# Kernel optimization log

Hardware: AMD Instinct MI355X
Metric: run time of the kernel (lower is better)

The kernel has to match this reference:

```python
import jax, jax.numpy as jnp
import numpy as np

D = 256; NH = 8; NL = 4; NP = 4; DH = D // NH; DFFN = 1024; NQ = 900; BS = 4
SPATIAL = ((92, 92), (46, 46), (23, 23), (12, 12))  # (H, W) per level
LEVEL_START = (0, 8464, 10580, 11109)
S = sum(h * w for h, w in SPATIAL)  # 11253


def _ln(x, g, b):
    m = jnp.mean(x, -1, keepdims=True)
    v = jnp.var(x, -1, keepdims=True)
    return (x - m) / jnp.sqrt(v + 1e-5) * g + b


def setup_inputs() -> dict:
    key = jax.random.key(0)
    ks = jax.random.split(key, 24)
    p = lambda k, s: 0.02 * jax.random.normal(k, s, jnp.float32)
    return {
        "tgt": jax.random.normal(ks[0], (NQ, BS, D), jnp.float32),
        "tgt_query_pos": jax.random.normal(ks[1], (NQ, BS, D), jnp.float32),
        "tgt_reference_points": jax.random.uniform(ks[2], (NQ, BS, NL, 2), jnp.float32),
        "memory": jax.random.normal(ks[3], (S, BS, D), jnp.float32),
        "memory_spatial_shapes": jnp.array(SPATIAL, jnp.int32),
        "memory_level_start_index": jnp.array(LEVEL_START, jnp.int32),
        "in_proj_w": p(ks[4], (3 * D, D)), "in_proj_b": p(ks[5], (3 * D,)),
        "out_proj_w": p(ks[6], (D, D)), "out_proj_b": p(ks[7], (D,)),
        "off_w": p(ks[8], (NH * NL * NP * 2, D)), "off_b": p(ks[9], (NH * NL * NP * 2,)),
        "aw_w": p(ks[10], (NH * NL * NP, D)), "aw_b": p(ks[11], (NH * NL * NP,)),
        "vproj_w": p(ks[12], (D, D)), "vproj_b": p(ks[13], (D,)),
        "oproj_w": p(ks[14], (D, D)), "oproj_b": p(ks[15], (D,)),
        "ln1_g": jnp.ones((D,), jnp.float32), "ln1_b": jnp.zeros((D,), jnp.float32),
        "ln2_g": jnp.ones((D,), jnp.float32), "ln2_b": jnp.zeros((D,), jnp.float32),
        "ln3_g": jnp.ones((D,), jnp.float32), "ln3_b": jnp.zeros((D,), jnp.float32),
        "lin1_w": p(ks[16], (DFFN, D)), "lin1_b": p(ks[17], (DFFN,)),
        "lin2_w": p(ks[18], (D, DFFN)), "lin2_b": p(ks[19], (D,)),
    }


def _self_attn(q, k, v, in_w, in_b, out_w, out_b):
    # q, k, v: (nq, bs, d) -- torch nn.MultiheadAttention, eval mode
    wq, wk, wv = jnp.split(in_w, 3, axis=0)
    bq, bk, bv = jnp.split(in_b, 3)
    qp = (q @ wq.T + bq).reshape(NQ, BS, NH, DH)
    kp = (k @ wk.T + bk).reshape(NQ, BS, NH, DH)
    vp = (v @ wv.T + bv).reshape(NQ, BS, NH, DH)
    s = jnp.einsum("qbhd,kbhd->bhqk", qp, kp) / jnp.sqrt(jnp.float32(DH))
    a = jax.nn.softmax(s, axis=-1)
    o = jnp.einsum("bhqk,kbhd->qbhd", a, vp).reshape(NQ, BS, D)
    return o @ out_w.T + out_b


def _msdeform(x, ref, mem, off_w, off_b, aw_w, aw_b, vproj_w, vproj_b, oproj_w, oproj_b):
    # x: (bs, nq, d); ref: (bs, nq, nl, 2) in [0,1]; mem: (bs, S, d)
    value = (mem @ vproj_w.T + vproj_b).reshape(BS, S, NH, DH)
    off = (x @ off_w.T + off_b).reshape(BS, NQ, NH, NL, NP, 2)
    aw = jax.nn.softmax((x @ aw_w.T + aw_b).reshape(BS, NQ, NH, NL * NP), axis=-1)
    aw = aw.reshape(BS, NQ, NH, NL, NP)
    # offset normalizer = (W, H) per level
    norm = jnp.array([[w, h] for (h, w) in SPATIAL], jnp.float32)
    loc = ref[:, :, None, :, None, :] + off / norm[None, None, None, :, None, :]
    out = jnp.zeros((BS, NH, NQ, DH), x.dtype)
    for l, (H, W) in enumerate(SPATIAL):
        s0 = LEVEL_START[l]
        v = value[:, s0:s0 + H * W].transpose(0, 2, 1, 3)  # (bs, nh, H*W, dh)
        g = loc[:, :, :, l].transpose(0, 2, 1, 3, 4)       # (bs, nh, nq, np, 2)
        # grid_sample align_corners=False, padding_mode='zeros'
        px = g[..., 0] * W - 0.5
        py = g[..., 1] * H - 0.5
        x0 = jnp.floor(px).astype(jnp.int32)
        y0 = jnp.floor(py).astype(jnp.int32)
        wx = px - x0
        wy = py - y0
        samp = jnp.zeros((BS, NH, NQ, NP, DH), x.dtype)
        for dx, dy, w in ((0, 0, (1 - wx) * (1 - wy)), (1, 0, wx * (1 - wy)),
                          (0, 1, (1 - wx) * wy), (1, 1, wx * wy)):
            xi = x0 + dx
            yi = y0 + dy
            valid = ((xi >= 0) & (xi < W) & (yi >= 0) & (yi < H)).astype(x.dtype)
            idx = (jnp.clip(yi, 0, H - 1) * W + jnp.clip(xi, 0, W - 1)).reshape(BS, NH, NQ * NP)
            gat = jnp.take_along_axis(v, idx[..., None], axis=2).reshape(BS, NH, NQ, NP, DH)
            samp = samp + (w * valid)[..., None] * gat
        a = aw[:, :, :, l].transpose(0, 2, 1, 3)  # (bs, nh, nq, np)
        out = out + (samp * a[..., None]).sum(axis=3)
    out = out.transpose(0, 2, 1, 3).reshape(BS, NQ, D)
    return out @ oproj_w.T + oproj_b


def reference(tgt, tgt_query_pos, tgt_reference_points, memory,
              memory_spatial_shapes, memory_level_start_index,
              in_proj_w, in_proj_b, out_proj_w, out_proj_b,
              off_w, off_b, aw_w, aw_b, vproj_w, vproj_b, oproj_w, oproj_b,
              ln1_g, ln1_b, ln2_g, ln2_b, ln3_g, ln3_b,
              lin1_w, lin1_b, lin2_w, lin2_b):
    # module_seq = ['sa', 'ca', 'ffn']; dropout inactive (eval)
    q = tgt + tgt_query_pos
    tgt2 = _self_attn(q, q, tgt, in_proj_w, in_proj_b, out_proj_w, out_proj_b)
    tgt = _ln(tgt + tgt2, ln2_g, ln2_b)
    x = (tgt + tgt_query_pos).transpose(1, 0, 2)
    ref = tgt_reference_points.transpose(1, 0, 2, 3)
    mem = memory.transpose(1, 0, 2)
    tgt2 = _msdeform(x, ref, mem, off_w, off_b, aw_w, aw_b,
                     vproj_w, vproj_b, oproj_w, oproj_b).transpose(1, 0, 2)
    tgt = _ln(tgt + tgt2, ln1_g, ln1_b)
    ff = jax.nn.relu(tgt @ lin1_w.T + lin1_b) @ lin2_w.T + lin2_b
    return _ln(tgt + ff, ln3_g, ln3_b)
```

## Files before the change

### kernel.cpp

```cpp
#include <hip/hip_runtime.h>
#include <math.h>

#define D_MODEL 256
#define NHEAD   8
#define NLVL    4
#define NPTS    4
#define DHEAD   32
#define DFFN    1024
#define NQ      900
#define BSZ     4
#define NROW    (NQ * BSZ)
#define S_TOT   11253
#define VROWS   (S_TOT * BSZ)
#define SASCALE 0.17677669529663687f

typedef __attribute__((ext_vector_type(8))) short short8;
typedef __attribute__((ext_vector_type(4))) float f32x4;
typedef unsigned short ushort_t;

static __device__ __forceinline__ unsigned f2bf1(float f) {
    unsigned u = __float_as_uint(f);
    return (u + 0x7FFFu + ((u >> 16) & 1u)) >> 16;
}
static __device__ __forceinline__ unsigned pack2bf(float x, float y) {
    return f2bf1(x) | (f2bf1(y) << 16);
}
static __device__ __forceinline__ float bf2f(ushort_t u) {
    return __uint_as_float(((unsigned)u) << 16);
}

#define GPAD 72

__global__ __launch_bounds__(256) void qkv_fused(
    const float* __restrict__ tgt, const float* __restrict__ qpos,
    const float* __restrict__ W, const float* __restrict__ bias,
    ushort_t* __restrict__ C)
{
    __shared__ ushort_t As[64 * GPAD];
    __shared__ ushort_t Ws[64 * GPAD];

    const int t  = threadIdx.x;
    const int m0 = blockIdx.x * 64;
    const int n0 = blockIdx.y * 64;
    const bool addpos = (n0 < 512);
    const float oscale = (n0 < 256) ? SASCALE : 1.f;

    const int trow = t >> 2;
    const int tk   = (t & 3) << 4;
    const int wv   = t >> 6;
    const int ln   = t & 63;
    const int L    = ln & 15;
    const int quad = ln >> 4;

    f32x4 acc[4] = {{0.f,0.f,0.f,0.f},{0.f,0.f,0.f,0.f},
                    {0.f,0.f,0.f,0.f},{0.f,0.f,0.f,0.f}};

    for (int k0 = 0; k0 < 256; k0 += 64) {
        {
            int m = m0 + trow;
            float4 a0, a1, a2, a3;
            if (m < NROW) {
                const float* ap = tgt + (size_t)m * 256 + k0 + tk;
                a0 = *(const float4*)(ap + 0);
                a1 = *(const float4*)(ap + 4);
                a2 = *(const float4*)(ap + 8);
                a3 = *(const float4*)(ap + 12);
                if (addpos) {
                    const float* pp = qpos + (size_t)m * 256 + k0 + tk;
                    float4 p0 = *(const float4*)(pp + 0);
                    float4 p1 = *(const float4*)(pp + 4);
                    float4 p2 = *(const float4*)(pp + 8);
                    float4 p3 = *(const float4*)(pp + 12);
                    a0.x += p0.x; a0.y += p0.y; a0.z += p0.z; a0.w += p0.w;
                    a1.x += p1.x; a1.y += p1.y; a1.z += p1.z; a1.w += p1.w;
                    a2.x += p2.x; a2.y += p2.y; a2.z += p2.z; a2.w += p2.w;
                    a3.x += p3.x; a3.y += p3.y; a3.z += p3.z; a3.w += p3.w;
                }
            } else {
                a0 = a1 = a2 = a3 = make_float4(0.f, 0.f, 0.f, 0.f);
            }
            uint4 u0, u1;
            u0.x = pack2bf(a0.x, a0.y); u0.y = pack2bf(a0.z, a0.w);
            u0.z = pack2bf(a1.x, a1.y); u0.w = pack2bf(a1.z, a1.w);
            u1.x = pack2bf(a2.x, a2.y); u1.y = pack2bf(a2.z, a2.w);
            u1.z = pack2bf(a3.x, a3.y); u1.w = pack2bf(a3.z, a3.w);
            *(uint4*)&As[trow * GPAD + tk + 0] = u0;
            *(uint4*)&As[trow * GPAD + tk + 8] = u1;
        }
        {
            int n = n0 + trow;
            const float* wp = W + (size_t)n * 256 + k0 + tk;
            float4 a0 = *(const float4*)(wp + 0);
            float4 a1 = *(const float4*)(wp + 4);
            float4 a2 = *(const float4*)(wp + 8);
            float4 a3 = *(const float4*)(wp + 12);
            uint4 u0, u1;
            u0.x = pack2bf(a0.x, a0.y); u0.y = pack2bf(a0.z, a0.w);
            u0.z = pack2bf(a1.x, a1.y); u0.w = pack2bf(a1.z, a1.w);
            u1.x = pack2bf(a2.x, a2.y); u1.y = pack2bf(a2.z, a2.w);
            u1.z = pack2bf(a3.x, a3.y); u1.w = pack2bf(a3.z, a3.w);
            *(uint4*)&Ws[trow * GPAD + tk + 0] = u0;
            *(uint4*)&Ws[trow * GPAD + tk + 8] = u1;
        }
        __syncthreads();
#pragma unroll
        for (int kh = 0; kh < 2; ++kh) {
            short8 af = *(const short8*)&As[(wv * 16 + L) * GPAD + kh * 32 + quad * 8];
#pragma unroll
            for (int cb = 0; cb < 4; ++cb) {
                short8 bf = *(const short8*)&Ws[(cb * 16 + L) * GPAD + kh * 32 + quad * 8];
                acc[cb] = __builtin_amdgcn_mfma_f32_16x16x32_bf16(af, bf, acc[cb], 0, 0, 0);
            }
        }
        __syncthreads();
    }
#pragma unroll
    for (int cb = 0; cb < 4; ++cb) {
        int col = n0 + cb * 16 + L;
        float bv = bias[col];
#pragma unroll
        for (int i = 0; i < 4; ++i) {
            int m = m0 + wv * 16 + quad * 4 + i;
            if (m < NROW)
                C[(size_t)m * 768 + col] = (ushort_t)f2bf1((acc[cb][i] + bv) * oscale);
        }
    }
}

__global__ __launch_bounds__(256) void sa_flash16(
    const ushort_t* __restrict__ qkv, ushort_t* __restrict__ attn_out)
{
    __shared__ ushort_t Ks[2 * 2080];
    __shared__ ushort_t Vt[2 * 2304];
    __shared__ ushort_t Ps[4 * 1152];

    const int t    = threadIdx.x;
    const int q0   = blockIdx.x * 64;
    const int b    = blockIdx.y & 3;
    const int h    = blockIdx.y >> 2;
// ... 182 lines not shown
        __syncthreads();
    }
#pragma unroll
    for (int cb = 0; cb < 4; ++cb) {
        int col = n0 + cb * 16 + L;
        float bv = bias[col];
#pragma unroll
        for (int i = 0; i < 4; ++i) {
            int m = m0 + wv * 16 + quad * 4 + i;
            if (m < M)
                C[(size_t)m * ldc + col] = acc[cb][i] + bv;
        }
    }
}

__global__ __launch_bounds__(256) void ln_resid16(
    const float* __restrict__ xa, const float* __restrict__ xb,
    const float* __restrict__ gam, const float* __restrict__ bet,
    float* __restrict__ out, const float* __restrict__ pos,
    ushort_t* __restrict__ out2)
{
    const int row = blockIdx.x;
    const int t = threadIdx.x;
    float x = xa[(size_t)row * D_MODEL + t] + xb[(size_t)row * D_MODEL + t];
    float s = x, s2 = x * x;
#pragma unroll
    for (int off = 32; off > 0; off >>= 1) {
        s  += __shfl_down(s, off, 64);
        s2 += __shfl_down(s2, off, 64);
    }
    __shared__ float rs[4], rs2[4];
    __shared__ float mean_s, rstd_s;
    int wid = t >> 6, lane = t & 63;
    if (lane == 0) { rs[wid] = s; rs2[wid] = s2; }
    __syncthreads();
    if (t == 0) {
        float S = rs[0] + rs[1] + rs[2] + rs[3];
        float S2 = rs2[0] + rs2[1] + rs2[2] + rs2[3];
        float mean = S * (1.f / 256.f);
        float var = S2 * (1.f / 256.f) - mean * mean;
        mean_s = mean;
        rstd_s = rsqrtf(var + 1e-5f);
    }
    __syncthreads();
    float y = (x - mean_s) * rstd_s * gam[t] + bet[t];
    out[(size_t)row * D_MODEL + t] = y;
    if (out2) {
        float o2 = y + (pos ? pos[(size_t)row * D_MODEL + t] : 0.f);
        out2[(size_t)row * D_MODEL + t] = (ushort_t)f2bf1(o2);
    }
}

__global__ __launch_bounds__(256) void vproj_bf16(
    const float* __restrict__ A, const float* __restrict__ W,
    const float* __restrict__ bias, ushort_t* __restrict__ C, int M)
{
    __shared__ ushort_t As[64 * GPAD];
    __shared__ ushort_t Ws[256 * GPAD];

    const int t  = threadIdx.x;
    const int m0 = blockIdx.x * 64;
    const int trow = t >> 2;
    const int tk   = (t & 3) << 4;
    const int wv   = t >> 6;
    const int ln   = t & 63;
    const int L    = ln & 15;
    const int quad = ln >> 4;

    f32x4 acc[16];
#pragma unroll
    for (int i = 0; i < 16; ++i) acc[i] = (f32x4){0.f, 0.f, 0.f, 0.f};

    for (int k0 = 0; k0 < 256; k0 += 64) {
        {
            int m = m0 + trow;
            float4 a0, a1, a2, a3;
            if (m < M) {
                const float* ap = A + (size_t)m * 256 + k0 + tk;
                a0 = *(const float4*)(ap + 0);
                a1 = *(const float4*)(ap + 4);
                a2 = *(const float4*)(ap + 8);
                a3 = *(const float4*)(ap + 12);
            } else {
                a0 = a1 = a2 = a3 = make_float4(0.f, 0.f, 0.f, 0.f);
            }
            uint4 u0, u1;
            u0.x = pack2bf(a0.x, a0.y); u0.y = pack2bf(a0.z, a0.w);
            u0.z = pack2bf(a1.x, a1.y); u0.w = pack2bf(a1.z, a1.w);
            u1.x = pack2bf(a2.x, a2.y); u1.y = pack2bf(a2.z, a2.w);
            u1.z = pack2bf(a3.x, a3.y); u1.w = pack2bf(a3.z, a3.w);
            *(uint4*)&As[trow * GPAD + tk + 0] = u0;
            *(uint4*)&As[trow * GPAD + tk + 8] = u1;
        }
#pragma unroll
        for (int wb = 0; wb < 4; ++wb) {
            int n = wb * 64 + trow;
            const float* wp = W + (size_t)n * 256 + k0 + tk;
            float4 a0 = *(const float4*)(wp + 0);
            float4 a1 = *(const float4*)(wp + 4);
            float4 a2 = *(const float4*)(wp + 8);
            float4 a3 = *(const float4*)(wp + 12);
            uint4 u0, u1;
            u0.x = pack2bf(a0.x, a0.y); u0.y = pack2bf(a0.z, a0.w);
            u0.z = pack2bf(a1.x, a1.y); u0.w = pack2bf(a1.z, a1.w);
            u1.x = pack2bf(a2.x, a2.y); u1.y = pack2bf(a2.z, a2.w);
            u1.z = pack2bf(a3.x, a3.y); u1.w = pack2bf(a3.z, a3.w);
            *(uint4*)&Ws[n * GPAD + tk + 0] = u0;
            *(uint4*)&Ws[n * GPAD + tk + 8] = u1;
        }
        __syncthreads();
#pragma unroll
        for (int kh = 0; kh < 2; ++kh) {
            short8 af = *(const short8*)&As[(wv * 16 + L) * GPAD + kh * 32 + quad * 8];
#pragma unroll
            for (int cb = 0; cb < 16; ++cb) {
                short8 bf = *(const short8*)&Ws[(cb * 16 + L) * GPAD + kh * 32 + quad * 8];
                acc[cb] = __builtin_amdgcn_mfma_f32_16x16x32_bf16(af, bf, acc[cb], 0, 0, 0);
            }
        }
        __syncthreads();
    }

    ushort_t* Cs = Ws;
#pragma unroll
    for (int cb = 0; cb < 16; ++cb) {
        int col = cb * 16 + L;
        float bv = bias[col];
#pragma unroll
        for (int i = 0; i < 4; ++i) {
            int r = wv * 16 + quad * 4 + i;
            Cs[r * 264 + col] = (ushort_t)f2bf1(acc[cb][i] + bv);
        }
    }
    __syncthreads();
    {
        int r  = t >> 2;
        int ch = (t & 3) * 64;
        int m  = m0 + r;
        if (m < M) {
            const ushort_t* src = &Cs[r * 264 + ch];
            uint4* dst = (uint4*)(C + (size_t)m * 256 + ch);
#pragma unroll
            for (int j = 0; j < 8; ++j)
                dst[j] = *(const uint4*)(src + j * 8);
        }
    }
}

__global__ __launch_bounds__(256) void offaw16(
    const ushort_t* __restrict__ A,
    const float* __restrict__ off_w, const float* __restrict__ off_b,
    const float* __restrict__ aw_w, const float* __restrict__ aw_b,
    float* __restrict__ off_raw, float* __restrict__ aw_raw)
{
    __shared__ ushort_t As[64 * GPAD];
    __shared__ ushort_t Ws[64 * GPAD];

    const int t  = threadIdx.x;
    const int m0 = blockIdx.x * 64;
    const int by = blockIdx.y;
    const bool isaw = (by >= 4);
    const int n0 = isaw ? (by - 4) * 64 : by * 64;
    const float* W  = isaw ? aw_w : off_w;
    const float* bs = isaw ? aw_b : off_b;
    float* C = isaw ? aw_raw : off_raw;
    const int ldc = isaw ? 128 : 256;

    const int trow = t >> 2;
    const int tk   = (t & 3) << 4;
    const int wv   = t >> 6;
    const int ln   = t & 63;
    const int L    = ln & 15;
    const int quad = ln >> 4;

    f32x4 acc[4] = {{0.f,0.f,0.f,0.f},{0.f,0.f,0.f,0.f},
                    {0.f,0.f,0.f,0.f},{0.f,0.f,0.f,0.f}};

    for (int k0 = 0; k0 < 256; k0 += 64) {
        {
            int m = m0 + trow;
            uint4 a0 = make_uint4(0u,0u,0u,0u), a1 = make_uint4(0u,0u,0u,0u);
            if (m < NROW) {
                const ushort_t* ap = A + (size_t)m * 256 + k0 + tk;
                a0 = *(const uint4*)ap;
                a1 = *(const uint4*)(ap + 8);
            }
            *(uint4*)&As[trow * GPAD + tk + 0] = a0;
            *(uint4*)&As[trow * GPAD + tk + 8] = a1;
        }
        {
            int n = n0 + trow;
            const float* wp = W + (size_t)n * 256 + k0 + tk;
            float4 a0 = *(const float4*)(wp + 0);
            float4 a1 = *(const float4*)(wp + 4);
            float4 a2 = *(const float4*)(wp + 8);
            float4 a3 = *(const float4*)(wp + 12);
            uint4 u0, u1;
            u0.x = pack2bf(a0.x, a0.y); u0.y = pack2bf(a0.z, a0.w);
            u0.z = pack2bf(a1.x, a1.y); u0.w = pack2bf(a1.z, a1.w);
            u1.x = pack2bf(a2.x, a2.y); u1.y = pack2bf(a2.z, a2.w);
            u1.z = pack2bf(a3.x, a3.y); u1.w = pack2bf(a3.z, a3.w);
            *(uint4*)&Ws[trow * GPAD + tk + 0] = u0;
            *(uint4*)&Ws[trow * GPAD + tk + 8] = u1;
        }
        __syncthreads();
#pragma unroll
        for (int kh = 0; kh < 2; ++kh) {
            short8 af = *(const short8*)&As[(wv * 16 + L) * GPAD + kh * 32 + quad * 8];
#pragma unroll
            for (int cb = 0; cb < 4; ++cb) {
                short8 bf = *(const short8*)&Ws[(cb * 16 + L) * GPAD + kh * 32 + quad * 8];
                acc[cb] = __builtin_amdgcn_mfma_f32_16x16x32_bf16(af, bf, acc[cb], 0, 0, 0);
            }
        }
        __syncthreads();
    }
#pragma unroll
    for (int cb = 0; cb < 4; ++cb) {
        int col = n0 + cb * 16 + L;
        float bv = bs[col];
#pragma unroll
        for (int i = 0; i < 4; ++i) {
            int m = m0 + wv * 16 + quad * 4 + i;
            if (m < NROW)
                C[(size_t)m * ldc + col] = acc[cb][i] + bv;
        }
    }
}

__global__ __launch_bounds__(256) void gemm16_16(
    const ushort_t* __restrict__ A, const float* __restrict__ W,
    const float* __restrict__ bias, ushort_t* __restrict__ C,
    int M, int N, int K, int ldc, int relu)
{
    __shared__ ushort_t As[64 * GPAD];
    __shared__ ushort_t Ws[64 * GPAD];

    const int t  = threadIdx.x;
    const int m0 = blockIdx.x * 64;
    const int n0 = blockIdx.y * 64;
    const int trow = t >> 2;
    const int tk   = (t & 3) << 4;
    const int wv   = t >> 6;
    const int ln   = t & 63;
    const int L    = ln & 15;
    const int quad = ln >> 4;

    f32x4 acc[4] = {{0.f,0.f,0.f,0.f},{0.f,0.f,0.f,0.f},
                    {0.f,0.f,0.f,0.f},{0.f,0.f,0.f,0.f}};

    for (int k0 = 0; k0 < K; k0 += 64) {
        {
            int m = m0 + trow;
            uint4 a0 = make_uint4(0u,0u,0u,0u), a1 = make_uint4(0u,0u,0u,0u);
            if (m < M) {
                const ushort_t* ap = A + (size_t)m * K + k0 + tk;
                a0 = *(const uint4*)ap;
                a1 = *(const uint4*)(ap + 8);
            }
            *(uint4*)&As[trow * GPAD + tk + 0] = a0;
            *(uint4*)&As[trow * GPAD + tk + 8] = a1;
        }
        {
            int n = n0 + trow;
            const float* wp = W + (size_t)n * K + k0 + tk;
            float4 a0 = *(const float4*)(wp + 0);
            float4 a1 = *(const float4*)(wp + 4);
            float4 a2 = *(const float4*)(wp + 8);
            float4 a3 = *(const float4*)(wp + 12);
            uint4 u0, u1;
            u0.x = pack2bf(a0.x, a0.y); u0.y = pack2bf(a0.z, a0.w);
            u0.z = pack2bf(a1.x, a1.y); u0.w = pack2bf(a1.z, a1.w);
            u1.x = pack2bf(a2.x, a2.y); u1.y = pack2bf(a2.z, a2.w);
            u1.z = pack2bf(a3.x, a3.y); u1.w = pack2bf(a3.z, a3.w);
            *(uint4*)&Ws[trow * GPAD + tk + 0] = u0;
            *(uint4*)&Ws[trow * GPAD + tk + 8] = u1;
        }
        __syncthreads();
#pragma unroll
        for (int kh = 0; kh < 2; ++kh) {
            short8 af = *(const short8*)&As[(wv * 16 + L) * GPAD + kh * 32 + quad * 8];
#pragma unroll
            for (int cb = 0; cb < 4; ++cb) {
                short8 bf = *(const short8*)&Ws[(cb * 16 + L) * GPAD + kh * 32 + quad * 8];
                acc[cb] = __builtin_amdgcn_mfma_f32_16x16x32_bf16(af, bf, acc[cb], 0, 0, 0);
            }
        }
        __syncthreads();
    }
#pragma unroll
    for (int cb = 0; cb < 4; ++cb) {
        int col = n0 + cb * 16 + L;
        float bv = bias[col];
#pragma unroll
        for (int i = 0; i < 4; ++i) {
            int m = m0 + wv * 16 + quad * 4 + i;
            if (m < M) {
                float o = acc[cb][i] + bv;
                if (relu) o = fmaxf(o, 0.f);
                C[(size_t)m * ldc + col] = (ushort_t)f2bf1(o);
            }
        }
    }
}

__global__ __launch_bounds__(256) void msdeform16(
    const float* __restrict__ off_raw, const float* __restrict__ aw_raw,
    const float* __restrict__ refp, const ushort_t* __restrict__ value,
    ushort_t* __restrict__ out)
{
    const int row = blockIdx.x;
    const int b = row & 3;
    const int t = threadIdx.x;

    __shared__ float aw_s[8][17];
    __shared__ float px_s[8][16];
    __shared__ float py_s[8][16];

// ... 82 lines not shown
    const float* op_w   = (const float*)d_in[16];
    const float* op_b   = (const float*)d_in[17];
    const float* ln1g   = (const float*)d_in[18];
    const float* ln1b   = (const float*)d_in[19];
    const float* ln2g   = (const float*)d_in[20];
    const float* ln2b   = (const float*)d_in[21];
    const float* ln3g   = (const float*)d_in[22];
    const float* ln3b   = (const float*)d_in[23];
    const float* l1w    = (const float*)d_in[24];
    const float* l1b    = (const float*)d_in[25];
    const float* l2w    = (const float*)d_in[26];
    const float* l2b    = (const float*)d_in[27];
    float* out = (float*)d_out;
    float* ws  = (float*)d_ws;

    ushort_t* qkv16   = (ushort_t*)ws;
    ushort_t* att16   = (ushort_t*)(ws + 1382400);
    float*    tgt_a   = ws + 1843200;
    ushort_t* xca16   = (ushort_t*)(ws + 2764800);
    float*    off_raw = ws + 3225600;
    float*    aw_raw  = ws + 4147200;
    ushort_t* att2_16 = (ushort_t*)(ws + 4608000);
    float*    tgt_b   = ws + 5068800;
    ushort_t* tgtb16  = (ushort_t*)(ws + 5990400);
    ushort_t* value16 = (ushort_t*)(ws + 6451200);
    ushort_t* hidden16= (ushort_t*)(ws + 12212736);
    float*    tmp     = ws + 14055936;

    dim3 b256(256);

    hipLaunchKernelGGL(qkv_fused, dim3(57, 12), b256, 0, stream,
                       tgt, qpos, in_w, in_b, qkv16);
    hipLaunchKernelGGL(sa_flash16, dim3(15, 32), b256, 0, stream, qkv16, att16);
    hipLaunchKernelGGL(gemm16_f32, dim3(57, 4), b256, 0, stream,
                       att16, outp_w, outp_b, tmp, NROW, 256, 256, 256);
    hipLaunchKernelGGL(ln_resid16, dim3(3600), b256, 0, stream,
                       tgt, tmp, ln2g, ln2b, tgt_a, qpos, xca16);
    hipLaunchKernelGGL(vproj_bf16, dim3(704), b256, 0, stream,
                       mem, vp_w, vp_b, value16, VROWS);
    hipLaunchKernelGGL(offaw16, dim3(57, 6), b256, 0, stream,
                       xca16, off_w, off_b, aw_w, aw_b, off_raw, aw_raw);
    hipLaunchKernelGGL(msdeform16, dim3(3600), b256, 0, stream,
                       off_raw, aw_raw, refp, value16, att2_16);
    hipLaunchKernelGGL(gemm16_f32, dim3(57, 4), b256, 0, stream,
                       att2_16, op_w, op_b, tmp, NROW, 256, 256, 256);
    hipLaunchKernelGGL(ln_resid16, dim3(3600), b256, 0, stream,
                       tgt_a, tmp, ln1g, ln1b, tgt_b, (const float*)nullptr, tgtb16);
    hipLaunchKernelGGL(gemm16_16, dim3(57, 16), b256, 0, stream,
                       tgtb16, l1w, l1b, hidden16, NROW, 1024, 256, 1024, 1);
    hipLaunchKernelGGL(gemm16_f32, dim3(57, 4), b256, 0, stream,
                       hidden16, l2w, l2b, tmp, NROW, 256, 1024, 256);
    hipLaunchKernelGGL(ln_resid16, dim3(3600), b256, 0, stream,
                       tgt_b, tmp, ln3g, ln3b, out, (const float*)nullptr, (ushort_t*)nullptr);
}
```

Measured before the change: 290.9 us.

## Fuse QKV and value projections; fold LayerNorms into following GEMM prologues

Merges the QKV projection and the memory value projection into one launch, with the block index picking which GEMM a block runs. The LayerNorm after self-attention is fused into the offset/attention-weight GEMM, and the LayerNorm after cross-attention is fused into the first FFN GEMM. Each GEMM block computes the row LN itself and stages the normalized bf16 rows in shared memory, removing two kernel launches and the intermediate bf16 buffers. In exchange, the LN is recomputed by every column block (6x and 16x redundant reads of tgt and tmp), and the fused kernels use more shared memory.

```diff
diff --git a/kernel.cpp b/kernel.cpp
--- a/kernel.cpp
+++ b/kernel.cpp
@@ -31,20 +31,18 @@
 
 #define GPAD 72
 
-__global__ __launch_bounds__(256) void qkv_fused(
+__global__ __launch_bounds__(256) void proj_fused(
     const float* __restrict__ tgt, const float* __restrict__ qpos,
-    const float* __restrict__ W, const float* __restrict__ bias,
-    ushort_t* __restrict__ C)
+    const float* __restrict__ in_w, const float* __restrict__ in_b,
+    const float* __restrict__ mem, const float* __restrict__ vp_w,
+    const float* __restrict__ vp_b,
+    ushort_t* __restrict__ qkv16, ushort_t* __restrict__ value16)
 {
     __shared__ ushort_t As[64 * GPAD];
-    __shared__ ushort_t Ws[64 * GPAD];
-
-    const int t  = threadIdx.x;
-    const int m0 = blockIdx.x * 64;
-    const int n0 = blockIdx.y * 64;
-    const bool addpos = (n0 < 512);
-    const float oscale = (n0 < 256) ? SASCALE : 1.f;
-
+    __shared__ ushort_t Ws[256 * GPAD];
+
+    const int t    = threadIdx.x;
+    const int bid  = blockIdx.x;
     const int trow = t >> 2;
     const int tk   = (t & 3) << 4;
     const int wv   = t >> 6;
@@ -52,77 +50,165 @@
     const int L    = ln & 15;
     const int quad = ln >> 4;
 
-    f32x4 acc[4] = {{0.f,0.f,0.f,0.f},{0.f,0.f,0.f,0.f},
-                    {0.f,0.f,0.f,0.f},{0.f,0.f,0.f,0.f}};
-
-    for (int k0 = 0; k0 < 256; k0 += 64) {
+    if (bid < 684) {
+        const int m0 = (bid % 57) * 64;
+        const int n0 = (bid / 57) * 64;
+        const bool addpos = (n0 < 512);
+        const float oscale = (n0 < 256) ? SASCALE : 1.f;
+
+        f32x4 acc[4] = {{0.f,0.f,0.f,0.f},{0.f,0.f,0.f,0.f},
+                        {0.f,0.f,0.f,0.f},{0.f,0.f,0.f,0.f}};
+
+        for (int k0 = 0; k0 < 256; k0 += 64) {
+            {
+                int m = m0 + trow;
+                float4 a0, a1, a2, a3;
+                if (m < NROW) {
+                    const float* ap = tgt + (size_t)m * 256 + k0 + tk;
+                    a0 = *(const float4*)(ap + 0);
+                    a1 = *(const float4*)(ap + 4);
+                    a2 = *(const float4*)(ap + 8);
+                    a3 = *(const float4*)(ap + 12);
+                    if (addpos) {
+                        const float* pp = qpos + (size_t)m * 256 + k0 + tk;
+                        float4 p0 = *(const float4*)(pp + 0);
+                        float4 p1 = *(const float4*)(pp + 4);
+                        float4 p2 = *(const float4*)(pp + 8);
+                        float4 p3 = *(const float4*)(pp + 12);
+                        a0.x += p0.x; a0.y += p0.y; a0.z += p0.z; a0.w += p0.w;
+                        a1.x += p1.x; a1.y += p1.y; a1.z += p1.z; a1.w += p1.w;
+                        a2.x += p2.x; a2.y += p2.y; a2.z += p2.z; a2.w += p2.w;
+                        a3.x += p3.x; a3.y += p3.y; a3.z += p3.z; a3.w += p3.w;
+                    }
+                } else {
+                    a0 = a1 = a2 = a3 = make_float4(0.f, 0.f, 0.f, 0.f);
+                }
+                uint4 u0, u1;
+                u0.x = pack2bf(a0.x, a0.y); u0.y = pack2bf(a0.z, a0.w);
+                u0.z = pack2bf(a1.x, a1.y); u0.w = pack2bf(a1.z, a1.w);
+                u1.x = pack2bf(a2.x, a2.y); u1.y = pack2bf(a2.z, a2.w);
+                u1.z = pack2bf(a3.x, a3.y); u1.w = pack2bf(a3.z, a3.w);
+                *(uint4*)&As[trow * GPAD + tk + 0] = u0;
+                *(uint4*)&As[trow * GPAD + tk + 8] = u1;
+            }
+            {
+                int n = n0 + trow;
+                const float* wp = in_w + (size_t)n * 256 + k0 + tk;
+                float4 a0 = *(const float4*)(wp + 0);
+                float4 a1 = *(const float4*)(wp + 4);
+                float4 a2 = *(const float4*)(wp + 8);
+                float4 a3 = *(const float4*)(wp + 12);
+                uint4 u0, u1;
+                u0.x = pack2bf(a0.x, a0.y); u0.y = pack2bf(a0.z, a0.w);
+                u0.z = pack2bf(a1.x, a1.y); u0.w = pack2bf(a1.z, a1.w);
+                u1.x = pack2bf(a2.x, a2.y); u1.y = pack2bf(a2.z, a2.w);
+                u1.z = pack2bf(a3.x, a3.y); u1.w = pack2bf(a3.z, a3.w);
+                *(uint4*)&Ws[trow * GPAD + tk + 0] = u0;
+                *(uint4*)&Ws[trow * GPAD + tk + 8] = u1;
+            }
+            __syncthreads();
+#pragma unroll
+            for (int kh = 0; kh < 2; ++kh) {
+                short8 af = *(const short8*)&As[(wv * 16 + L) * GPAD + kh * 32 + quad * 8];
+#pragma unroll
+                for (int cb = 0; cb < 4; ++cb) {
+                    short8 bf = *(const short8*)&Ws[(cb * 16 + L) * GPAD + kh * 32 + quad * 8];
+                    acc[cb] = __builtin_amdgcn_mfma_f32_16x16x32_bf16(af, bf, acc[cb], 0, 0, 0);
+                }
+            }
+            __syncthreads();
+        }
+#pragma unroll
+        for (int cb = 0; cb < 4; ++cb) {
+            int col = n0 + cb * 16 + L;
+            float bv = in_b[col];
+#pragma unroll
+            for (int i = 0; i < 4; ++i) {
+                int m = m0 + wv * 16 + quad * 4 + i;
+                if (m < NROW)
+                    qkv16[(size_t)m * 768 + col] = (ushort_t)f2bf1((acc[cb][i] + bv) * oscale);
+            }
+        }
+    } else {
+        const int m0 = (bid - 684) * 64;
+
+        f32x4 acc[16];
+#pragma unroll
+        for (int i = 0; i < 16; ++i) acc[i] = (f32x4){0.f, 0.f, 0.f, 0.f};
+
+        for (int k0 = 0; k0 < 256; k0 += 64) {
+            {
+                int m = m0 + trow;
+                float4 a0, a1, a2, a3;
+                if (m < VROWS) {
+                    const float* ap = mem + (size_t)m * 256 + k0 + tk;
+                    a0 = *(const float4*)(ap + 0);
+                    a1 = *(const float4*)(ap + 4);
+                    a2 = *(const float4*)(ap + 8);
+                    a3 = *(const float4*)(ap + 12);
+                } else {
+                    a0 = a1 = a2 = a3 = make_float4(0.f, 0.f, 0.f, 0.f);
+                }
+                uint4 u0, u1;
+                u0.x = pack2bf(a0.x, a0.y); u0.y = pack2bf(a0.z, a0.w);
+                u0.z = pack2bf(a1.x, a1.y); u0.w = pack2bf(a1.z, a1.w);
+                u1.x = pack2bf(a2.x, a2.y); u1.y = pack2bf(a2.z, a2.w);
+                u1.z = pack2bf(a3.x, a3.y); u1.w = pack2bf(a3.z, a3.w);
+                *(uint4*)&As[trow * GPAD + tk + 0] = u0;
+                *(uint4*)&As[trow * GPAD + tk + 8] = u1;
+            }
+#pragma unroll
+            for (int wb = 0; wb < 4; ++wb) {
+                int n = wb * 64 + trow;
+                const float* wp = vp_w + (size_t)n * 256 + k0 + tk;
+                float4 a0 = *(const float4*)(wp + 0);
+                float4 a1 = *(const float4*)(wp + 4);
+                float4 a2 = *(const float4*)(wp + 8);
+                float4 a3 = *(const float4*)(wp + 12);
+                uint4 u0, u1;
+                u0.x = pack2bf(a0.x, a0.y); u0.y = pack2bf(a0.z, a0.w);
+                u0.z = pack2bf(a1.x, a1.y); u0.w = pack2bf(a1.z, a1.w);
+                u1.x = pack2bf(a2.x, a2.y); u1.y = pack2bf(a2.z, a2.w);
+                u1.z = pack2bf(a3.x, a3.y); u1.w = pack2bf(a3.z, a3.w);
+                *(uint4*)&Ws[n * GPAD + tk + 0] = u0;
+                *(uint4*)&Ws[n * GPAD + tk + 8] = u1;
+            }
+            __syncthreads();
+#pragma unroll
+            for (int kh = 0; kh < 2; ++kh) {
+                short8 af = *(const short8*)&As[(wv * 16 + L) * GPAD + kh * 32 + quad * 8];
+#pragma unroll
+                for (int cb = 0; cb < 16; ++cb) {
+                    short8 bf = *(const short8*)&Ws[(cb * 16 + L) * GPAD + kh * 32 + quad * 8];
+                    acc[cb] = __builtin_amdgcn_mfma_f32_16x16x32_bf16(af, bf, acc[cb], 0, 0, 0);
+                }
+            }
+            __syncthreads();
+        }
+
+        ushort_t* Cs = Ws;
+#pragma unroll
+        for (int cb = 0; cb < 16; ++cb) {
+            int col = cb * 16 + L;
+            float bv = vp_b[col];
+#pragma unroll
+            for (int i = 0; i < 4; ++i) {
+                int r = wv * 16 + quad * 4 + i;
+                Cs[r * 264 + col] = (ushort_t)f2bf1(acc[cb][i] + bv);
+            }
+        }
+        __syncthreads();
         {
-            int m = m0 + trow;
-            float4 a0, a1, a2, a3;
-            if (m < NROW) {
-                const float* ap = tgt + (size_t)m * 256 + k0 + tk;
-                a0 = *(const float4*)(ap + 0);
-                a1 = *(const float4*)(ap + 4);
-                a2 = *(const float4*)(ap + 8);
-                a3 = *(const float4*)(ap + 12);
-                if (addpos) {
-                    const float* pp = qpos + (size_t)m * 256 + k0 + tk;
-                    float4 p0 = *(const float4*)(pp + 0);
-                    float4 p1 = *(const float4*)(pp + 4);
-                    float4 p2 = *(const float4*)(pp + 8);
-                    float4 p3 = *(const float4*)(pp + 12);
-                    a0.x += p0.x; a0.y += p0.y; a0.z += p0.z; a0.w += p0.w;
-                    a1.x += p1.x; a1.y += p1.y; a1.z += p1.z; a1.w += p1.w;
-                    a2.x += p2.x; a2.y += p2.y; a2.z += p2.z; a2.w += p2.w;
-                    a3.x += p3.x; a3.y += p3.y; a3.z += p3.z; a3.w += p3.w;
-                }
-            } else {
-                a0 = a1 = a2 = a3 = make_float4(0.f, 0.f, 0.f, 0.f);
-            }
-            uint4 u0, u1;
-            u0.x = pack2bf(a0.x, a0.y); u0.y = pack2bf(a0.z, a0.w);
-            u0.z = pack2bf(a1.x, a1.y); u0.w = pack2bf(a1.z, a1.w);
-            u1.x = pack2bf(a2.x, a2.y); u1.y = pack2bf(a2.z, a2.w);
-            u1.z = pack2bf(a3.x, a3.y); u1.w = pack2bf(a3.z, a3.w);
-            *(uint4*)&As[trow * GPAD + tk + 0] = u0;
-            *(uint4*)&As[trow * GPAD + tk + 8] = u1;
-        }
-        {
-            int n = n0 + trow;
-            const float* wp = W + (size_t)n * 256 + k0 + tk;
-            float4 a0 = *(const float4*)(wp + 0);
-            float4 a1 = *(const float4*)(wp + 4);
-            float4 a2 = *(const float4*)(wp + 8);
-            float4 a3 = *(const float4*)(wp + 12);
-            uint4 u0, u1;
-            u0.x = pack2bf(a0.x, a0.y); u0.y = pack2bf(a0.z, a0.w);
-            u0.z = pack2bf(a1.x, a1.y); u0.w = pack2bf(a1.z, a1.w);
-            u1.x = pack2bf(a2.x, a2.y); u1.y = pack2bf(a2.z, a2.w);
-            u1.z = pack2bf(a3.x, a3.y); u1.w = pack2bf(a3.z, a3.w);
-            *(uint4*)&Ws[trow * GPAD + tk + 0] = u0;
-            *(uint4*)&Ws[trow * GPAD + tk + 8] = u1;
-        }
-        __syncthreads();
-#pragma unroll
-        for (int kh = 0; kh < 2; ++kh) {
-            short8 af = *(const short8*)&As[(wv * 16 + L) * GPAD + kh * 32 + quad * 8];
-#pragma unroll
-            for (int cb = 0; cb < 4; ++cb) {
-                short8 bf = *(const short8*)&Ws[(cb * 16 + L) * GPAD + kh * 32 + quad * 8];
-                acc[cb] = __builtin_amdgcn_mfma_f32_16x16x32_bf16(af, bf, acc[cb], 0, 0, 0);
-            }
-        }
-        __syncthreads();
-    }
-#pragma unroll
-    for (int cb = 0; cb < 4; ++cb) {
-        int col = n0 + cb * 16 + L;
-        float bv = bias[col];
-#pragma unroll
-        for (int i = 0; i < 4; ++i) {
-            int m = m0 + wv * 16 + quad * 4 + i;
-            if (m < NROW)
-                C[(size_t)m * 768 + col] = (ushort_t)f2bf1((acc[cb][i] + bv) * oscale);
+            int r  = t >> 2;
+            int ch = (t & 3) * 64;
+            int m  = m0 + r;
+            if (m < VROWS) {
+                const ushort_t* src = &Cs[r * 264 + ch];
+                uint4* dst = (uint4*)(value16 + (size_t)m * 256 + ch);
+#pragma unroll
+                for (int j = 0; j < 8; ++j)
+                    dst[j] = *(const uint4*)(src + j * 8);
+            }
         }
     }
 }
@@ -335,11 +421,247 @@
     }
 }
 
+__global__ __launch_bounds__(256) void offaw_ln(
+    const float* __restrict__ tgt, const float* __restrict__ tmp,
+    const float* __restrict__ qpos,
+    const float* __restrict__ gam, const float* __restrict__ bet,
+    const float* __restrict__ off_w, const float* __restrict__ off_b,
+    const float* __restrict__ aw_w, const float* __restrict__ aw_b,
+    float* __restrict__ off_raw, float* __restrict__ aw_raw,
+    float* __restrict__ tgt_a)
+{
+    __shared__ ushort_t Axc[4][64 * GPAD];
+    __shared__ ushort_t Ws[64 * GPAD];
+
+    const int t  = threadIdx.x;
+    const int m0 = blockIdx.x * 64;
+    const int by = blockIdx.y;
+    const bool isaw = (by >= 4);
+    const int n0 = isaw ? (by - 4) * 64 : by * 64;
+    const float* W  = isaw ? aw_w : off_w;
+    const float* bs = isaw ? aw_b : off_b;
+    float* C = isaw ? aw_raw : off_raw;
+    const int ldc = isaw ? 128 : 256;
+
+    const int wv   = t >> 6;
+    const int ln   = t & 63;
+    const int L    = ln & 15;
+    const int quad = ln >> 4;
+    const int trow = t >> 2;
+    const int tk   = (t & 3) << 4;
+
+    {
+        const int row = t >> 2, c4 = t & 3;
+        const int m = m0 + row;
+        const size_t base = (size_t)m * 256 + c4 * 64;
+        float s = 0.f, s2 = 0.f;
+        if (m < NROW) {
+#pragma unroll
+            for (int seg = 0; seg < 16; ++seg) {
+                float4 a = *(const float4*)(tgt + base + seg * 4);
+                float4 b = *(const float4*)(tmp + base + seg * 4);
+                float x0 = a.x + b.x, x1 = a.y + b.y;
+                float x2 = a.z + b.z, x3 = a.w + b.w;
+                s  += x0 + x1 + x2 + x3;
+                s2 += x0*x0 + x1*x1 + x2*x2 + x3*x3;
+            }
+        }
+        s  += __shfl_xor(s, 1, 64);  s  += __shfl_xor(s, 2, 64);
+        s2 += __shfl_xor(s2, 1, 64); s2 += __shfl_xor(s2, 2, 64);
+        float mean = s * (1.f / 256.f);
+        float var  = s2 * (1.f / 256.f) - mean * mean;
+        float rstd = rsqrtf(var + 1e-5f);
+        if (m < NROW) {
+#pragma unroll
+            for (int seg = 0; seg < 16; ++seg) {
+                int col = c4 * 64 + seg * 4;
+                float4 a = *(const float4*)(tgt + base + seg * 4);
+                float4 b = *(const float4*)(tmp + base + seg * 4);
+                float4 g = *(const float4*)(gam + col);
+                float4 be = *(const float4*)(bet + col);
+                float4 p = *(const float4*)(qpos + base + seg * 4);
+                float y0 = (a.x + b.x - mean) * rstd * g.x + be.x;
+                float y1 = (a.y + b.y - mean) * rstd * g.y + be.y;
+                float y2 = (a.z + b.z - mean) * rstd * g.z + be.z;
+                float y3 = (a.w + b.w - mean) * rstd * g.w + be.w;
+                if (by == 0)
+                    *(float4*)(tgt_a + base + seg * 4) = make_float4(y0, y1, y2, y3);
+                uint2 u;
+                u.x = pack2bf(y0 + p.x, y1 + p.y);
+                u.y = pack2bf(y2 + p.z, y3 + p.w);
+                *(uint2*)&Axc[c4][row * GPAD + seg * 4] = u;
+            }
+        } else {
+#pragma unroll
+            for (int seg = 0; seg < 16; ++seg)
+                *(uint2*)&Axc[c4][row * GPAD + seg * 4] = make_uint2(0u, 0u);
+        }
+    }
+    __syncthreads();
+
+    f32x4 acc[4] = {{0.f,0.f,0.f,0.f},{0.f,0.f,0.f,0.f},
+                    {0.f,0.f,0.f,0.f},{0.f,0.f,0.f,0.f}};
+
+    for (int kc = 0; kc < 4; ++kc) {
+        {
+            int n = n0 + trow;
+            const float* wp = W + (size_t)n * 256 + kc * 64 + tk;
+            float4 a0 = *(const float4*)(wp + 0);
+            float4 a1 = *(const float4*)(wp + 4);
+            float4 a2 = *(const float4*)(wp + 8);
+            float4 a3 = *(const float4*)(wp + 12);
+            uint4 u0, u1;
+            u0.x = pack2bf(a0.x, a0.y); u0.y = pack2bf(a0.z, a0.w);
+            u0.z = pack2bf(a1.x, a1.y); u0.w = pack2bf(a1.z, a1.w);
+            u1.x = pack2bf(a2.x, a2.y); u1.y = pack2bf(a2.z, a2.w);
+            u1.z = pack2bf(a3.x, a3.y); u1.w = pack2bf(a3.z, a3.w);
+            *(uint4*)&Ws[trow * GPAD + tk + 0] = u0;
+            *(uint4*)&Ws[trow * GPAD + tk + 8] = u1;
+        }
+        __syncthreads();
+#pragma unroll
+        for (int kh = 0; kh < 2; ++kh) {
+            short8 af = *(const short8*)&Axc[kc][(wv * 16 + L) * GPAD + kh * 32 + quad * 8];
+#pragma unroll
+            for (int cb = 0; cb < 4; ++cb) {
+                short8 bf = *(const short8*)&Ws[(cb * 16 + L) * GPAD + kh * 32 + quad * 8];
+                acc[cb] = __builtin_amdgcn_mfma_f32_16x16x32_bf16(af, bf, acc[cb], 0, 0, 0);
+            }
+        }
+        __syncthreads();
+    }
+#pragma unroll
+    for (int cb = 0; cb < 4; ++cb) {
+        int col = n0 + cb * 16 + L;
+        float bv = bs[col];
+#pragma unroll
+        for (int i = 0; i < 4; ++i) {
+            int m = m0 + wv * 16 + quad * 4 + i;
+            if (m < NROW)
+                C[(size_t)m * ldc + col] = acc[cb][i] + bv;
+        }
+    }
+}
+
+__global__ __launch_bounds__(256) void ffn1_ln(
+    const float* __restrict__ tgta, const float* __restrict__ tmp,
+    const float* __restrict__ gam, const float* __restrict__ bet,
+    const float* __restrict__ W, const float* __restrict__ bias,
+    ushort_t* __restrict__ hidden, float* __restrict__ tgt_b)
+{
+    __shared__ ushort_t Axc[4][64 * GPAD];
+    __shared__ ushort_t Ws[64 * GPAD];
+
+    const int t  = threadIdx.x;
+    const int m0 = blockIdx.x * 64;
+    const int by = blockIdx.y;
+    const int n0 = by * 64;
+
+    const int wv   = t >> 6;
+    const int ln   = t & 63;
+    const int L    = ln & 15;
+    const int quad = ln >> 4;
+    const int trow = t >> 2;
+    const int tk   = (t & 3) << 4;
+
+    {
+        const int row = t >> 2, c4 = t & 3;
+        const int m = m0 + row;
+        const size_t base = (size_t)m * 256 + c4 * 64;
+        float s = 0.f, s2 = 0.f;
+        if (m < NROW) {
+#pragma unroll
+            for (int seg = 0; seg < 16; ++seg) {
+                float4 a = *(const float4*)(tgta + base + seg * 4);
+                float4 b = *(const float4*)(tmp + base + seg * 4);
+                float x0 = a.x + b.x, x1 = a.y + b.y;
+                float x2 = a.z + b.z, x3 = a.w + b.w;
+                s  += x0 + x1 + x2 + x3;
+                s2 += x0*x0 + x1*x1 + x2*x2 + x3*x3;
+            }
+        }
+        s  += __shfl_xor(s, 1, 64);  s  += __shfl_xor(s, 2, 64);
+        s2 += __shfl_xor(s2, 1, 64); s2 += __shfl_xor(s2, 2, 64);
+        float mean = s * (1.f / 256.f);
+        float var  = s2 * (1.f / 256.f) - mean * mean;
+        float rstd = rsqrtf(var + 1e-5f);
+        if (m < NROW) {
+#pragma unroll
+            for (int seg = 0; seg < 16; ++seg) {
+                int col = c4 * 64 + seg * 4;
+                float4 a = *(const float4*)(tgta + base + seg * 4);
+                float4 b = *(const float4*)(tmp + base + seg * 4);
+                float4 g = *(const float4*)(gam + col);
+                float4 be = *(const float4*)(bet + col);
+                float y0 = (a.x + b.x - mean) * rstd * g.x + be.x;
+                float y1 = (a.y + b.y - mean) * rstd * g.y + be.y;
+                float y2 = (a.z + b.z - mean) * rstd * g.z + be.z;
+                float y3 = (a.w + b.w - mean) * rstd * g.w + be.w;
+                if (by == 0)
+                    *(float4*)(tgt_b + base + seg * 4) = make_float4(y0, y1, y2, y3);
+                uint2 u;
+                u.x = pack2bf(y0, y1);
+                u.y = pack2bf(y2, y3);
+                *(uint2*)&Axc[c4][row * GPAD + seg * 4] = u;
+            }
+        } else {
+#pragma unroll
+            for (int seg = 0; seg < 16; ++seg)
+                *(uint2*)&Axc[c4][row * GPAD + seg * 4] = make_uint2(0u, 0u);
+        }
+    }
+    __syncthreads();
+
+    f32x4 acc[4] = {{0.f,0.f,0.f,0.f},{0.f,0.f,0.f,0.f},
+                    {0.f,0.f,0.f,0.f},{0.f,0.f,0.f,0.f}};
+
+    for (int kc = 0; kc < 4; ++kc) {
+        {
+            int n = n0 + trow;
+            const float* wp = W + (size_t)n * 256 + kc * 64 + tk;
+            float4 a0 = *(const float4*)(wp + 0);
+            float4 a1 = *(const float4*)(wp + 4);
+            float4 a2 = *(const float4*)(wp + 8);
+            float4 a3 = *(const float4*)(wp + 12);
+            uint4 u0, u1;
+            u0.x = pack2bf(a0.x, a0.y); u0.y = pack2bf(a0.z, a0.w);
+            u0.z = pack2bf(a1.x, a1.y); u0.w = pack2bf(a1.z, a1.w);
+            u1.x = pack2bf(a2.x, a2.y); u1.y = pack2bf(a2.z, a2.w);
+            u1.z = pack2bf(a3.x, a3.y); u1.w = pack2bf(a3.z, a3.w);
+            *(uint4*)&Ws[trow * GPAD + tk + 0] = u0;
+            *(uint4*)&Ws[trow * GPAD + tk + 8] = u1;
+        }
+        __syncthreads();
+#pragma unroll
+        for (int kh = 0; kh < 2; ++kh) {
+            short8 af = *(const short8*)&Axc[kc][(wv * 16 + L) * GPAD + kh * 32 + quad * 8];
+#pragma unroll
+            for (int cb = 0; cb < 4; ++cb) {
+                short8 bf = *(const short8*)&Ws[(cb * 16 + L) * GPAD + kh * 32 + quad * 8];
+                acc[cb] = __builtin_amdgcn_mfma_f32_16x16x32_bf16(af, bf, acc[cb], 0, 0, 0);
+            }
+        }
+        __syncthreads();
+    }
+#pragma unroll
+    for (int cb = 0; cb < 4; ++cb) {
+        int col = n0 + cb * 16 + L;
+        float bv = bias[col];
+#pragma unroll
+        for (int i = 0; i < 4; ++i) {
+            int m = m0 + wv * 16 + quad * 4 + i;
+            if (m < NROW) {
+                float o = fmaxf(acc[cb][i] + bv, 0.f);
+                hidden[(size_t)m * 1024 + col] = (ushort_t)f2bf1(o);
+            }
+        }
+    }
+}
+
 __global__ __launch_bounds__(256) void ln_resid16(
     const float* __restrict__ xa, const float* __restrict__ xb,
     const float* __restrict__ gam, const float* __restrict__ bet,
-    float* __restrict__ out, const float* __restrict__ pos,
-    ushort_t* __restrict__ out2)
+    float* __restrict__ out)
 {
     const int row = blockIdx.x;
     const int t = threadIdx.x;
@@ -364,265 +686,7 @@
         rstd_s = rsqrtf(var + 1e-5f);
     }
     __syncthreads();
-    float y = (x - mean_s) * rstd_s * gam[t] + bet[t];
-    out[(size_t)row * D_MODEL + t] = y;
-    if (out2) {
-        float o2 = y + (pos ? pos[(size_t)row * D_MODEL + t] : 0.f);
-        out2[(size_t)row * D_MODEL + t] = (ushort_t)f2bf1(o2);
-    }
-}
-
-__global__ __launch_bounds__(256) void vproj_bf16(
-    const float* __restrict__ A, const float* __restrict__ W,
-    const float* __restrict__ bias, ushort_t* __restrict__ C, int M)
-{
-    __shared__ ushort_t As[64 * GPAD];
-    __shared__ ushort_t Ws[256 * GPAD];
-
-    const int t  = threadIdx.x;
-    const int m0 = blockIdx.x * 64;
-    const int trow = t >> 2;
-    const int tk   = (t & 3) << 4;
-    const int wv   = t >> 6;
-    const int ln   = t & 63;
-    const int L    = ln & 15;
-    const int quad = ln >> 4;
-
-    f32x4 acc[16];
-#pragma unroll
-    for (int i = 0; i < 16; ++i) acc[i] = (f32x4){0.f, 0.f, 0.f, 0.f};
-
-    for (int k0 = 0; k0 < 256; k0 += 64) {
-        {
-            int m = m0 + trow;
-            float4 a0, a1, a2, a3;
-            if (m < M) {
-                const float* ap = A + (size_t)m * 256 + k0 + tk;
-                a0 = *(const float4*)(ap + 0);
-                a1 = *(const float4*)(ap + 4);
-                a2 = *(const float4*)(ap + 8);
-                a3 = *(const float4*)(ap + 12);
-            } else {
-                a0 = a1 = a2 = a3 = make_float4(0.f, 0.f, 0.f, 0.f);
-            }
-            uint4 u0, u1;
-            u0.x = pack2bf(a0.x, a0.y); u0.y = pack2bf(a0.z, a0.w);
-            u0.z = pack2bf(a1.x, a1.y); u0.w = pack2bf(a1.z, a1.w);
-            u1.x = pack2bf(a2.x, a2.y); u1.y = pack2bf(a2.z, a2.w);
-            u1.z = pack2bf(a3.x, a3.y); u1.w = pack2bf(a3.z, a3.w);
-            *(uint4*)&As[trow * GPAD + tk + 0] = u0;
-            *(uint4*)&As[trow * GPAD + tk + 8] = u1;
-        }
-#pragma unroll
-        for (int wb = 0; wb < 4; ++wb) {
-            int n = wb * 64 + trow;
-            const float* wp = W + (size_t)n * 256 + k0 + tk;
-            float4 a0 = *(const float4*)(wp + 0);
-            float4 a1 = *(const float4*)(wp + 4);
-            float4 a2 = *(const float4*)(wp + 8);
-            float4 a3 = *(const float4*)(wp + 12);
-            uint4 u0, u1;
-            u0.x = pack2bf(a0.x, a0.y); u0.y = pack2bf(a0.z, a0.w);
-            u0.z = pack2bf(a1.x, a1.y); u0.w = pack2bf(a1.z, a1.w);
-            u1.x = pack2bf(a2.x, a2.y); u1.y = pack2bf(a2.z, a2.w);
-            u1.z = pack2bf(a3.x, a3.y); u1.w = pack2bf(a3.z, a3.w);
-            *(uint4*)&Ws[n * GPAD + tk + 0] = u0;
-            *(uint4*)&Ws[n * GPAD + tk + 8] = u1;
-        }
-        __syncthreads();
-#pragma unroll
-        for (int kh = 0; kh < 2; ++kh) {
-            short8 af = *(const short8*)&As[(wv * 16 + L) * GPAD + kh * 32 + quad * 8];
-#pragma unroll
-            for (int cb = 0; cb < 16; ++cb) {
-                short8 bf = *(const short8*)&Ws[(cb * 16 + L) * GPAD + kh * 32 + quad * 8];
-                acc[cb] = __builtin_amdgcn_mfma_f32_16x16x32_bf16(af, bf, acc[cb], 0, 0, 0);
-            }
-        }
-        __syncthreads();
-    }
-
-    ushort_t* Cs = Ws;
-#pragma unroll
-    for (int cb = 0; cb < 16; ++cb) {
-        int col = cb * 16 + L;
-        float bv = bias[col];
-#pragma unroll
-        for (int i = 0; i < 4; ++i) {
-            int r = wv * 16 + quad * 4 + i;
-            Cs[r * 264 + col] = (ushort_t)f2bf1(acc[cb][i] + bv);
-        }
-    }
-    __syncthreads();
-    {
-        int r  = t >> 2;
-        int ch = (t & 3) * 64;
-        int m  = m0 + r;
-        if (m < M) {
-            const ushort_t* src = &Cs[r * 264 + ch];
-            uint4* dst = (uint4*)(C + (size_t)m * 256 + ch);
-#pragma unroll
-            for (int j = 0; j < 8; ++j)
-                dst[j] = *(const uint4*)(src + j * 8);
-        }
-    }
-}
-
-__global__ __launch_bounds__(256) void offaw16(
-    const ushort_t* __restrict__ A,
-    const float* __restrict__ off_w, const float* __restrict__ off_b,
-    const float* __restrict__ aw_w, const float* __restrict__ aw_b,
-    float* __restrict__ off_raw, float* __restrict__ aw_raw)
-{
-    __shared__ ushort_t As[64 * GPAD];
-    __shared__ ushort_t Ws[64 * GPAD];
-
-    const int t  = threadIdx.x;
-    const int m0 = blockIdx.x * 64;
-    const int by = blockIdx.y;
-    const bool isaw = (by >= 4);
-    const int n0 = isaw ? (by - 4) * 64 : by * 64;
-    const float* W  = isaw ? aw_w : off_w;
-    const float* bs = isaw ? aw_b : off_b;
-    float* C = isaw ? aw_raw : off_raw;
-    const int ldc = isaw ? 128 : 256;
-
-    const int trow = t >> 2;
-    const int tk   = (t & 3) << 4;
-    const int wv   = t >> 6;
-    const int ln   = t & 63;
-    const int L    = ln & 15;
-    const int quad = ln >> 4;
-
-    f32x4 acc[4] = {{0.f,0.f,0.f,0.f},{0.f,0.f,0.f,0.f},
-                    {0.f,0.f,0.f,0.f},{0.f,0.f,0.f,0.f}};
-
-    for (int k0 = 0; k0 < 256; k0 += 64) {
-        {
-            int m = m0 + trow;
-            uint4 a0 = make_uint4(0u,0u,0u,0u), a1 = make_uint4(0u,0u,0u,0u);
-            if (m < NROW) {
-                const ushort_t* ap = A + (size_t)m * 256 + k0 + tk;
-                a0 = *(const uint4*)ap;
-                a1 = *(const uint4*)(ap + 8);
-            }
-            *(uint4*)&As[trow * GPAD + tk + 0] = a0;
-            *(uint4*)&As[trow * GPAD + tk + 8] = a1;
-        }
-        {
-            int n = n0 + trow;
-            const float* wp = W + (size_t)n * 256 + k0 + tk;
-            float4 a0 = *(const float4*)(wp + 0);
-            float4 a1 = *(const float4*)(wp + 4);
-            float4 a2 = *(const float4*)(wp + 8);
-            float4 a3 = *(const float4*)(wp + 12);
-            uint4 u0, u1;
-            u0.x = pack2bf(a0.x, a0.y); u0.y = pack2bf(a0.z, a0.w);
-            u0.z = pack2bf(a1.x, a1.y); u0.w = pack2bf(a1.z, a1.w);
-            u1.x = pack2bf(a2.x, a2.y); u1.y = pack2bf(a2.z, a2.w);
-            u1.z = pack2bf(a3.x, a3.y); u1.w = pack2bf(a3.z, a3.w);
-            *(uint4*)&Ws[trow * GPAD + tk + 0] = u0;
-            *(uint4*)&Ws[trow * GPAD + tk + 8] = u1;
-        }
-        __syncthreads();
-#pragma unroll
-        for (int kh = 0; kh < 2; ++kh) {
-            short8 af = *(const short8*)&As[(wv * 16 + L) * GPAD + kh * 32 + quad * 8];
-#pragma unroll
-            for (int cb = 0; cb < 4; ++cb) {
-                short8 bf = *(const short8*)&Ws[(cb * 16 + L) * GPAD + kh * 32 + quad * 8];
-                acc[cb] = __builtin_amdgcn_mfma_f32_16x16x32_bf16(af, bf, acc[cb], 0, 0, 0);
-            }
-        }
-        __syncthreads();
-    }
-#pragma unroll
-    for (int cb = 0; cb < 4; ++cb) {
-        int col = n0 + cb * 16 + L;
-        float bv = bs[col];
-#pragma unroll
-        for (int i = 0; i < 4; ++i) {
-            int m = m0 + wv * 16 + quad * 4 + i;
-            if (m < NROW)
-                C[(size_t)m * ldc + col] = acc[cb][i] + bv;
-        }
-    }
-}
-
-__global__ __launch_bounds__(256) void gemm16_16(
-    const ushort_t* __restrict__ A, const float* __restrict__ W,
-    const float* __restrict__ bias, ushort_t* __restrict__ C,
-    int M, int N, int K, int ldc, int relu)
-{
-    __shared__ ushort_t As[64 * GPAD];
-    __shared__ ushort_t Ws[64 * GPAD];
-
-    const int t  = threadIdx.x;
-    const int m0 = blockIdx.x * 64;
-    const int n0 = blockIdx.y * 64;
-    const int trow = t >> 2;
-    const int tk   = (t & 3) << 4;
-    const int wv   = t >> 6;
-    const int ln   = t & 63;
-    const int L    = ln & 15;
-    const int quad = ln >> 4;
-
-    f32x4 acc[4] = {{0.f,0.f,0.f,0.f},{0.f,0.f,0.f,0.f},
-                    {0.f,0.f,0.f,0.f},{0.f,0.f,0.f,0.f}};
-
-    for (int k0 = 0; k0 < K; k0 += 64) {
-        {
-            int m = m0 + trow;
-            uint4 a0 = make_uint4(0u,0u,0u,0u), a1 = make_uint4(0u,0u,0u,0u);
-            if (m < M) {
-                const ushort_t* ap = A + (size_t)m * K + k0 + tk;
-                a0 = *(const uint4*)ap;
-                a1 = *(const uint4*)(ap + 8);
-            }
-            *(uint4*)&As[trow * GPAD + tk + 0] = a0;
-            *(uint4*)&As[trow * GPAD + tk + 8] = a1;
-        }
-        {
-            int n = n0 + trow;
-            const float* wp = W + (size_t)n * K + k0 + tk;
-            float4 a0 = *(const float4*)(wp + 0);
-            float4 a1 = *(const float4*)(wp + 4);
-            float4 a2 = *(const float4*)(wp + 8);
-            float4 a3 = *(const float4*)(wp + 12);
-            uint4 u0, u1;
-            u0.x = pack2bf(a0.x, a0.y); u0.y = pack2bf(a0.z, a0.w);
-            u0.z = pack2bf(a1.x, a1.y); u0.w = pack2bf(a1.z, a1.w);
-            u1.x = pack2bf(a2.x, a2.y); u1.y = pack2bf(a2.z, a2.w);
-            u1.z = pack2bf(a3.x, a3.y); u1.w = pack2bf(a3.z, a3.w);
-            *(uint4*)&Ws[trow * GPAD + tk + 0] = u0;
-            *(uint4*)&Ws[trow * GPAD + tk + 8] = u1;
-        }
-        __syncthreads();
-#pragma unroll
-        for (int kh = 0; kh < 2; ++kh) {
-            short8 af = *(const short8*)&As[(wv * 16 + L) * GPAD + kh * 32 + quad * 8];
-#pragma unroll
-            for (int cb = 0; cb < 4; ++cb) {
-                short8 bf = *(const short8*)&Ws[(cb * 16 + L) * GPAD + kh * 32 + quad * 8];
-                acc[cb] = __builtin_amdgcn_mfma_f32_16x16x32_bf16(af, bf, acc[cb], 0, 0, 0);
-            }
-        }
-        __syncthreads();
-    }
-#pragma unroll
-    for (int cb = 0; cb < 4; ++cb) {
-        int col = n0 + cb * 16 + L;
-        float bv = bias[col];
-#pragma unroll
-        for (int i = 0; i < 4; ++i) {
-            int m = m0 + wv * 16 + quad * 4 + i;
-            if (m < M) {
-                float o = acc[cb][i] + bv;
-                if (relu) o = fmaxf(o, 0.f);
-                C[(size_t)m * ldc + col] = (ushort_t)f2bf1(o);
-            }
-        }
-    }
+    out[(size_t)row * D_MODEL + t] = (x - mean_s) * rstd_s * gam[t] + bet[t];
 }
 
 __global__ __launch_bounds__(256) void msdeform16(
@@ -735,42 +799,35 @@
     float* out = (float*)d_out;
     float* ws  = (float*)d_ws;
 
-    ushort_t* qkv16   = (ushort_t*)ws;
-    ushort_t* att16   = (ushort_t*)(ws + 1382400);
-    float*    tgt_a   = ws + 1843200;
-    ushort_t* xca16   = (ushort_t*)(ws + 2764800);
-    float*    off_raw = ws + 3225600;
-    float*    aw_raw  = ws + 4147200;
-    ushort_t* att2_16 = (ushort_t*)(ws + 4608000);
-    float*    tgt_b   = ws + 5068800;
-    ushort_t* tgtb16  = (ushort_t*)(ws + 5990400);
-    ushort_t* value16 = (ushort_t*)(ws + 6451200);
-    ushort_t* hidden16= (ushort_t*)(ws + 12212736);
-    float*    tmp     = ws + 14055936;
+    ushort_t* qkv16    = (ushort_t*)ws;
+    ushort_t* att16    = (ushort_t*)(ws + 691200);
+    float*    tmp      = ws + 921600;
+    float*    tgt_a    = ws + 1843200;
+    float*    off_raw  = ws + 2764800;
+    float*    aw_raw   = ws + 3686400;
+    ushort_t* att2_16  = (ushort_t*)(ws + 4147200);
+    float*    tgt_b    = ws + 4377600;
+    ushort_t* value16  = (ushort_t*)(ws + 5299200);
+    ushort_t* hidden16 = (ushort_t*)(ws + 11060736);
 
     dim3 b256(256);
 
-    hipLaunchKernelGGL(qkv_fused, dim3(57, 12), b256, 0, stream,
-                       tgt, qpos, in_w, in_b, qkv16);
+    hipLaunchKernelGGL(proj_fused, dim3(1388), b256, 0, stream,
+                       tgt, qpos, in_w, in_b, mem, vp_w, vp_b, qkv16, value16);
     hipLaunchKernelGGL(sa_flash16, dim3(15, 32), b256, 0, stream, qkv16, att16);
     hipLaunchKernelGGL(gemm16_f32, dim3(57, 4), b256, 0, stream,
                        att16, outp_w, outp_b, tmp, NROW, 256, 256, 256);
-    hipLaunchKernelGGL(ln_resid16, dim3(3600), b256, 0, stream,
-                       tgt, tmp, ln2g, ln2b, tgt_a, qpos, xca16);
-    hipLaunchKernelGGL(vproj_bf16, dim3(704), b256, 0, stream,
-                       mem, vp_w, vp_b, value16, VROWS);
-    hipLaunchKernelGGL(offaw16, dim3(57, 6), b256, 0, stream,
-                       xca16, off_w, off_b, aw_w, aw_b, off_raw, aw_raw);
+    hipLaunchKernelGGL(offaw_ln, dim3(57, 6), b256, 0, stream,
+                       tgt, tmp, qpos, ln2g, ln2b,
+                       off_w, off_b, aw_w, aw_b, off_raw, aw_raw, tgt_a);
     hipLaunchKernelGGL(msdeform16, dim3(3600), b256, 0, stream,
                        off_raw, aw_raw, refp, value16, att2_16);
     hipLaunchKernelGGL(gemm16_f32, dim3(57, 4), b256, 0, stream,
                        att2_16, op_w, op_b, tmp, NROW, 256, 256, 256);
-    hipLaunchKernelGGL(ln_resid16, dim3(3600), b256, 0, stream,
-                       tgt_a, tmp, ln1g, ln1b, tgt_b, (const float*)nullptr, tgtb16);
-    hipLaunchKernelGGL(gemm16_16, dim3(57, 16), b256, 0, stream,
-                       tgtb16, l1w, l1b, hidden16, NROW, 1024, 256, 1024, 1);
+    hipLaunchKernelGGL(ffn1_ln, dim3(57, 16), b256, 0, stream,
+                       tgt_a, tmp, ln1g, ln1b, l1w, l1b, hidden16, tgt_b);
     hipLaunchKernelGGL(gemm16_f32, dim3(57, 4), b256, 0, stream,
                        hidden16, l2w, l2b, tmp, NROW, 256, 1024, 256);
     hipLaunchKernelGGL(ln_resid16, dim3(3600), b256, 0, stream,
-                       tgt_b, tmp, ln3g, ln3b, out, (const float*)nullptr, (ushort_t*)nullptr);
-}
+                       tgt_b, tmp, ln3g, ln3b, out);
+}
```

After: 405.9 us. 39.5% more time.
